# Kernel tuning notes

Measured on AMD Instinct MI355X. Metric: run time of the kernel, lower is better.

The kernel has to match this reference:

```python
import jax, jax.numpy as jnp
import numpy as np
from jax import lax

N, T, K = 20000, 512, 12  # K = num_factors + 4


def setup_inputs() -> dict:
    key = jax.random.key(0)
    k1, k2, k3 = jax.random.split(key, 3)
    y = jax.random.normal(k1, (N, T), dtype=jnp.float32)
    f = jax.random.normal(k2, (T, K - 4), dtype=jnp.float32)
    # GARCH params must satisfy omega>0, a+b<1 for stationarity; scale uniforms
    theta = jax.random.uniform(k3, (N, T + 1, K), dtype=jnp.float32) * 0.4 + 0.01
    return {"y": y, "f": f, "theta": theta}


def reference(y, f, theta):
    th = theta[:, 1:, :]                      # [N, T, K]
    a = th[:, :, -3]                          # [N, T]
    b = th[:, :, -2]
    omega = th[:, :, -1]
    a_plus_b = a + b
    # epsilon = y - intercept - sum_f loadings * factors
    eps = y - th[:, :, 0] - jnp.einsum('ntf,tf->nt', th[:, :, 1:-3], f)
    eps2 = jnp.square(eps)
    # unconditional-variance init
    sigma2_0 = omega[:, 0] + a_plus_b[:, 0] * (
        jnp.mean(omega, axis=1) / (1.0 - jnp.mean(a_plus_b, axis=1)))
    # recurrence sigma2[t] = omega[t] + a[t]*sigma2[t-1] + b[t]*eps2[t-1]
    xs = (omega[:, 1:].T, a[:, 1:].T, b[:, 1:].T, eps2[:, :-1].T)  # time-major [T-1, N]

    def step(s, x):
        o_t, a_t, b_t, e_t = x
        s_new = o_t + a_t * s + b_t * e_t
        return s_new, s_new

    _, rest = lax.scan(step, sigma2_0, xs)    # rest: [T-1, N]
    sigma2 = jnp.concatenate([sigma2_0[:, None], rest.T], axis=1)  # [N, T]
    loss = jnp.mean(eps2 / sigma2 + jnp.log(sigma2))
    return (loss, eps, sigma2)
```

## Files before the change

### kernel.cpp

```cpp
#include <hip/hip_runtime.h>

#define N_ROWS 20000
#define T_DIM  512
#define K_DIM  12
#define TH_ROW ((T_DIM + 1) * K_DIM)
#define NBLK   (N_ROWS / 4)

__device__ __forceinline__ float fast_rcp(float x) { return __builtin_amdgcn_rcpf(x); }

__device__ __forceinline__ int tads(int tl) { return 9 * (tl >> 3) + (tl & 7); }

__device__ __forceinline__ void scan_chunk(
    const float* __restrict__ la, const float* __restrict__ lb,
    const float* __restrict__ lo, const float* __restrict__ le,
    int lane, int c, float s0, float& s_carry, float& e2_carry,
    float* __restrict__ sig_row, float& lsum)
{
    const int base = 9 * (lane >> 1) + 4 * (lane & 1);
    float av[4], bv[4], ov[4], e2v[4];
    #pragma unroll
    for (int i = 0; i < 4; ++i) {
        av[i] = la[base + i]; bv[i] = lb[base + i];
        ov[i] = lo[base + i]; e2v[i] = le[base + i];
    }
    float ep0 = e2_carry;
    if (lane > 0) ep0 = le[tads(4 * lane - 1)];

    float cv[4];
    cv[0] = fmaf(bv[0], ep0,    ov[0]);
    cv[1] = fmaf(bv[1], e2v[0], ov[1]);
    cv[2] = fmaf(bv[2], e2v[1], ov[2]);
    cv[3] = fmaf(bv[3], e2v[2], ov[3]);
    if (c == 0 && lane == 0) { av[0] = 0.f; cv[0] = s0; }

    float A = av[0], B = cv[0];
    #pragma unroll
    for (int i = 1; i < 4; ++i) { B = fmaf(av[i], B, cv[i]); A = av[i] * A; }

    float sA = A, sB = B;
    #pragma unroll
    for (int d = 1; d < 64; d <<= 1) {
        float Ap = __shfl_up(sA, d);
        float Bp = __shfl_up(sB, d);
        if (lane >= d) { sB = fmaf(sA, Bp, sB); sA = sA * Ap; }
    }
    float exA = __shfl_up(sA, 1), exB = __shfl_up(sB, 1);
    if (lane == 0) { exA = 1.f; exB = 0.f; }
    float s = fmaf(exA, s_carry, exB);

    #pragma unroll
    for (int i = 0; i < 4; ++i) {
        s = fmaf(av[i], s, cv[i]);
        sig_row[c * 256 + 4 * lane + i] = s;
        lsum += e2v[i] * fast_rcp(s) + __logf(s);
    }
    s_carry  = __shfl(s, 63);
    e2_carry = __shfl(e2v[3], 63);
}

__global__ __launch_bounds__(256) void garch_kernel(
    const float* __restrict__ y,
    const float* __restrict__ f,
    const float* __restrict__ theta,
    float* __restrict__ ws_part,
    float* __restrict__ out_eps,
    float* __restrict__ out_sig)
{
    __shared__ float lds_f[T_DIM * 9];
    __shared__ float lds_scan[4][4 * 288];
    __shared__ float lds_part[4];

    const int tid = threadIdx.x;
    for (int idx = tid; idx < T_DIM * 8; idx += 256) {
        int t = idx >> 3, j = idx & 7;
        lds_f[t * 9 + j] = f[idx];
    }
    __syncthreads();

    const int wave = tid >> 6;
    const int lane = tid & 63;
    const int n = blockIdx.x * 4 + wave;

    float* const wb = &lds_scan[wave][0];
    float* const la = wb;
    float* const lb = wb + 288;
    float* const lo = wb + 576;
    float* const le = wb + 864;

    const float* th_row = theta + (size_t)n * TH_ROW;
    const float* y_row  = y + (size_t)n * T_DIM;
    float* eps_row = out_eps + (size_t)n * T_DIM;
    float* sig_row = out_sig + (size_t)n * T_DIM;

    float a1[4], b1[4], o1[4], e1[4];
    float osum = 0.f, absum = 0.f;

    float4 pv0[4], pv1[4], pv2[4];
    float  py[4];
    #pragma unroll
    for (int i = 0; i < 4; ++i) {
        const int t = i * 64 + lane;
        const float4* p = (const float4*)(th_row + (size_t)(t + 1) * K_DIM);
        pv0[i] = p[0]; pv1[i] = p[1]; pv2[i] = p[2];
        py[i]  = y_row[t];
    }

    #pragma unroll
    for (int i = 0; i < 8; ++i) {
        const int slot = i & 3;
        const int t = i * 64 + lane;
        const float4 v0 = pv0[slot], v1 = pv1[slot], v2 = pv2[slot];
        const float  yv = py[slot];
        if (i < 4) {
            const int t2 = (i + 4) * 64 + lane;
            const float4* p = (const float4*)(th_row + (size_t)(t2 + 1) * K_DIM);
            pv0[slot] = p[0]; pv1[slot] = p[1]; pv2[slot] = p[2];
            py[slot]  = y_row[t2];
        }
        const float* fp = &lds_f[t * 9];
        float eps = yv - v0.x;
        eps = fmaf(-v0.y, fp[0], eps);
        eps = fmaf(-v0.z, fp[1], eps);
        eps = fmaf(-v0.w, fp[2], eps);
        eps = fmaf(-v1.x, fp[3], eps);
        eps = fmaf(-v1.y, fp[4], eps);
        eps = fmaf(-v1.z, fp[5], eps);
        eps = fmaf(-v1.w, fp[6], eps);
        eps = fmaf(-v2.x, fp[7], eps);
        eps_row[t] = eps;
        const float e2 = eps * eps;
        osum  += v2.w;
        absum += v2.y + v2.z;
        if (i < 4) {
            const int ad = tads(t);
            la[ad] = v2.y; lb[ad] = v2.z; lo[ad] = v2.w; le[ad] = e2;
        } else {
            a1[slot] = v2.y; b1[slot] = v2.z; o1[slot] = v2.w; e1[slot] = e2;
        }
    }

    #pragma unroll
    for (int d = 32; d; d >>= 1) {
        osum  += __shfl_xor(osum, d);
        absum += __shfl_xor(absum, d);
    }
    const float omean  = osum  * (1.0f / 512.0f);
    const float abmean = absum * (1.0f / 512.0f);
    const float s0 = lo[0] + (la[0] + lb[0]) * (omean / (1.0f - abmean));

    float s_carry = 0.f, e2_carry = 0.f, lsum = 0.f;
    scan_chunk(la, lb, lo, le, lane, 0, s0, s_carry, e2_carry, sig_row, lsum);

    #pragma unroll
    for (int i = 0; i < 4; ++i) {
        const int tl = i * 64 + lane;
        const int ad = tads(tl);
        la[ad] = a1[i]; lb[ad] = b1[i]; lo[ad] = o1[i]; le[ad] = e1[i];
    }
    scan_chunk(la, lb, lo, le, lane, 1, s0, s_carry, e2_carry, sig_row, lsum);

    #pragma unroll
    for (int d = 32; d; d >>= 1) lsum += __shfl_xor(lsum, d);
    if (lane == 0) lds_part[wave] = lsum;
    __syncthreads();
    if (tid == 0) {
        ws_part[blockIdx.x] = lds_part[0] + lds_part[1] + lds_part[2] + lds_part[3];
    }
}

__global__ __launch_bounds__(1024) void reduce_kernel(
    const float* __restrict__ ws_part, float* __restrict__ out_loss)
{
    __shared__ float w[16];
    float s = 0.f;
    for (int i = threadIdx.x; i < NBLK; i += 1024) s += ws_part[i];
    #pragma unroll
    for (int d = 32; d; d >>= 1) s += __shfl_xor(s, d);
    const int wave = threadIdx.x >> 6, lane = threadIdx.x & 63;
    if (lane == 0) w[wave] = s;
    __syncthreads();
    if (threadIdx.x == 0) {
        float t = 0.f;
        #pragma unroll
        for (int i = 0; i < 16; ++i) t += w[i];
        out_loss[0] = t * (1.0f / ((float)N_ROWS * (float)T_DIM));
    }
}

extern "C" void kernel_launch(void* const* d_in, const int* in_sizes, int n_in,
                              void* d_out, int out_size, void* d_ws, size_t ws_size,
                              hipStream_t stream) {
    const float* y     = (const float*)d_in[0];
    const float* f     = (const float*)d_in[1];
    const float* theta = (const float*)d_in[2];
    float* out = (float*)d_out;
    float* ws  = (float*)d_ws;

    float* out_eps = out + 1;
    float* out_sig = out + 1 + (size_t)N_ROWS * T_DIM;

    garch_kernel<<<NBLK, 256, 0, stream>>>(y, f, theta, ws, out_eps, out_sig);
    reduce_kernel<<<1, 1024, 0, stream>>>(ws, out);
}
```

Baseline: 125.7 us.

## Precompute recurrence constant in registers and shrink LDS scan staging

Computes c[t] = omega[t] + b[t]*eps2[t-1] in the load loop, using a lane shuffle to get the previous eps2, so only a and c go through LDS instead of four arrays. The f table moves to a factor-major LDS layout, and the scan reads eps back from the just-written global output instead of LDS. A launch-bounds occupancy hint of 6 is added. Together these cut LDS footprint and traffic, which should allow more resident waves, at the cost of a global re-read of eps and a few extra shuffles.

```diff
diff --git a/kernel.cpp b/kernel.cpp
--- a/kernel.cpp
+++ b/kernel.cpp
@@ -11,27 +11,21 @@
 __device__ __forceinline__ int tads(int tl) { return 9 * (tl >> 3) + (tl & 7); }
 
 __device__ __forceinline__ void scan_chunk(
-    const float* __restrict__ la, const float* __restrict__ lb,
-    const float* __restrict__ lo, const float* __restrict__ le,
-    int lane, int c, float s0, float& s_carry, float& e2_carry,
-    float* __restrict__ sig_row, float& lsum)
+    const float* __restrict__ la, const float* __restrict__ lc,
+    const float* __restrict__ eps_c,
+    int lane, bool first, float s0, float& s_carry,
+    float* __restrict__ sig_c, float& lsum)
 {
     const int base = 9 * (lane >> 1) + 4 * (lane & 1);
-    float av[4], bv[4], ov[4], e2v[4];
-    #pragma unroll
-    for (int i = 0; i < 4; ++i) {
-        av[i] = la[base + i]; bv[i] = lb[base + i];
-        ov[i] = lo[base + i]; e2v[i] = le[base + i];
-    }
-    float ep0 = e2_carry;
-    if (lane > 0) ep0 = le[tads(4 * lane - 1)];
-
-    float cv[4];
-    cv[0] = fmaf(bv[0], ep0,    ov[0]);
-    cv[1] = fmaf(bv[1], e2v[0], ov[1]);
-    cv[2] = fmaf(bv[2], e2v[1], ov[2]);
-    cv[3] = fmaf(bv[3], e2v[2], ov[3]);
-    if (c == 0 && lane == 0) { av[0] = 0.f; cv[0] = s0; }
+    float av[4], cv[4], e2v[4];
+    #pragma unroll
+    for (int i = 0; i < 4; ++i) {
+        float e = eps_c[4 * lane + i];
+        e2v[i] = e * e;
+        av[i] = la[base + i];
+        cv[i] = lc[base + i];
+    }
+    if (first && lane == 0) { av[0] = 0.f; cv[0] = s0; }
 
     float A = av[0], B = cv[0];
     #pragma unroll
@@ -51,14 +45,13 @@
     #pragma unroll
     for (int i = 0; i < 4; ++i) {
         s = fmaf(av[i], s, cv[i]);
-        sig_row[c * 256 + 4 * lane + i] = s;
+        sig_c[4 * lane + i] = s;
         lsum += e2v[i] * fast_rcp(s) + __logf(s);
     }
-    s_carry  = __shfl(s, 63);
-    e2_carry = __shfl(e2v[3], 63);
-}
-
-__global__ __launch_bounds__(256) void garch_kernel(
+    s_carry = __shfl(s, 63);
+}
+
+__global__ __launch_bounds__(256, 6) void garch_kernel(
     const float* __restrict__ y,
     const float* __restrict__ f,
     const float* __restrict__ theta,
@@ -66,14 +59,14 @@
     float* __restrict__ out_eps,
     float* __restrict__ out_sig)
 {
-    __shared__ float lds_f[T_DIM * 9];
-    __shared__ float lds_scan[4][4 * 288];
+    __shared__ float lds_f[8][T_DIM];
+    __shared__ float lds_ac[4][2 * 288];
     __shared__ float lds_part[4];
 
     const int tid = threadIdx.x;
     for (int idx = tid; idx < T_DIM * 8; idx += 256) {
-        int t = idx >> 3, j = idx & 7;
-        lds_f[t * 9 + j] = f[idx];
+        const int j = idx >> 9, t = idx & 511;
+        lds_f[j][t] = f[t * 8 + j];
     }
     __syncthreads();
 
@@ -81,19 +74,18 @@
     const int lane = tid & 63;
     const int n = blockIdx.x * 4 + wave;
 
-    float* const wb = &lds_scan[wave][0];
-    float* const la = wb;
-    float* const lb = wb + 288;
-    float* const lo = wb + 576;
-    float* const le = wb + 864;
+    float* const la = &lds_ac[wave][0];
+    float* const lc = &lds_ac[wave][288];
 
     const float* th_row = theta + (size_t)n * TH_ROW;
     const float* y_row  = y + (size_t)n * T_DIM;
     float* eps_row = out_eps + (size_t)n * T_DIM;
     float* sig_row = out_sig + (size_t)n * T_DIM;
 
-    float a1[4], b1[4], o1[4], e1[4];
+    float a1[4], c1[4];
     float osum = 0.f, absum = 0.f;
+    float last_e2 = 0.f;
+    float a0 = 0.f, b0 = 0.f, o0 = 0.f;
 
     float4 pv0[4], pv1[4], pv2[4];
     float  py[4];
@@ -117,25 +109,33 @@
             pv0[slot] = p[0]; pv1[slot] = p[1]; pv2[slot] = p[2];
             py[slot]  = y_row[t2];
         }
-        const float* fp = &lds_f[t * 9];
         float eps = yv - v0.x;
-        eps = fmaf(-v0.y, fp[0], eps);
-        eps = fmaf(-v0.z, fp[1], eps);
-        eps = fmaf(-v0.w, fp[2], eps);
-        eps = fmaf(-v1.x, fp[3], eps);
-        eps = fmaf(-v1.y, fp[4], eps);
-        eps = fmaf(-v1.z, fp[5], eps);
-        eps = fmaf(-v1.w, fp[6], eps);
-        eps = fmaf(-v2.x, fp[7], eps);
+        eps = fmaf(-v0.y, lds_f[0][t], eps);
+        eps = fmaf(-v0.z, lds_f[1][t], eps);
+        eps = fmaf(-v0.w, lds_f[2][t], eps);
+        eps = fmaf(-v1.x, lds_f[3][t], eps);
+        eps = fmaf(-v1.y, lds_f[4][t], eps);
+        eps = fmaf(-v1.z, lds_f[5][t], eps);
+        eps = fmaf(-v1.w, lds_f[6][t], eps);
+        eps = fmaf(-v2.x, lds_f[7][t], eps);
         eps_row[t] = eps;
         const float e2 = eps * eps;
+
+        float ep = __shfl_up(e2, 1);
+        if (lane == 0) ep = last_e2;
+        last_e2 = __shfl(e2, 63);
+
+        const float cc = fmaf(v2.z, ep, v2.w);
         osum  += v2.w;
         absum += v2.y + v2.z;
+        if (i == 0) {
+            a0 = __shfl(v2.y, 0); b0 = __shfl(v2.z, 0); o0 = __shfl(v2.w, 0);
+        }
         if (i < 4) {
             const int ad = tads(t);
-            la[ad] = v2.y; lb[ad] = v2.z; lo[ad] = v2.w; le[ad] = e2;
+            la[ad] = v2.y; lc[ad] = cc;
         } else {
-            a1[slot] = v2.y; b1[slot] = v2.z; o1[slot] = v2.w; e1[slot] = e2;
+            a1[slot] = v2.y; c1[slot] = cc;
         }
     }
 
@@ -146,18 +146,17 @@
     }
     const float omean  = osum  * (1.0f / 512.0f);
     const float abmean = absum * (1.0f / 512.0f);
-    const float s0 = lo[0] + (la[0] + lb[0]) * (omean / (1.0f - abmean));
-
-    float s_carry = 0.f, e2_carry = 0.f, lsum = 0.f;
-    scan_chunk(la, lb, lo, le, lane, 0, s0, s_carry, e2_carry, sig_row, lsum);
-
-    #pragma unroll
-    for (int i = 0; i < 4; ++i) {
-        const int tl = i * 64 + lane;
-        const int ad = tads(tl);
-        la[ad] = a1[i]; lb[ad] = b1[i]; lo[ad] = o1[i]; le[ad] = e1[i];
-    }
-    scan_chunk(la, lb, lo, le, lane, 1, s0, s_carry, e2_carry, sig_row, lsum);
+    const float s0 = o0 + (a0 + b0) * (omean / (1.0f - abmean));
+
+    float s_carry = 0.f, lsum = 0.f;
+    scan_chunk(la, lc, eps_row, lane, true, s0, s_carry, sig_row, lsum);
+
+    #pragma unroll
+    for (int i = 0; i < 4; ++i) {
+        const int ad = tads(i * 64 + lane);
+        la[ad] = a1[i]; lc[ad] = c1[i];
+    }
+    scan_chunk(la, lc, eps_row + 256, lane, false, s0, s_carry, sig_row + 256, lsum);
 
     #pragma unroll
     for (int d = 32; d; d >>= 1) lsum += __shfl_xor(lsum, d);
```

Measured after the change: 180.2 us. +43.3%, slower.
